# Performance work log

Measured on AMD Instinct MI355X. Metric: run time of the kernel, lower is better.

Reference implementation:

```python
import jax, jax.numpy as jnp
import numpy as np

N = 50000
E_RAND = 800000
F_IN = 128
H = 4          # num_heads
D_HID = 32     # hidden per-head dim
D_OUT = 32     # output per-head dim
NEG_SLOPE_ATTN = 0.2   # DGL GATConv attention leaky_relu
NEG_SLOPE_ACT = 0.01   # F.leaky_relu default activation


def setup_inputs() -> dict:
    key = jax.random.key(0)
    ks = jax.random.split(key, 12)
    x = jax.random.normal(ks[0], (N, F_IN), dtype=jnp.float32)
    src_r = jax.random.randint(ks[1], (E_RAND,), 0, N, dtype=jnp.int32)
    dst_r = jax.random.randint(ks[2], (E_RAND,), 0, N, dtype=jnp.int32)
    loop = jnp.arange(N, dtype=jnp.int32)
    src = jnp.concatenate([src_r, loop])  # add_self_loop
    dst = jnp.concatenate([dst_r, loop])
    sc1 = 1.0 / np.sqrt(F_IN)
    sc2 = 1.0 / np.sqrt(H * D_HID)
    W1 = jax.random.normal(ks[3], (F_IN, H * D_HID), dtype=jnp.float32) * sc1
    al1 = jax.random.normal(ks[4], (H, D_HID), dtype=jnp.float32) * sc1
    ar1 = jax.random.normal(ks[5], (H, D_HID), dtype=jnp.float32) * sc1
    b1 = jnp.zeros((H * D_HID,), dtype=jnp.float32)
    W2 = jax.random.normal(ks[6], (H * D_HID, H * D_OUT), dtype=jnp.float32) * sc2
    al2 = jax.random.normal(ks[7], (H, D_OUT), dtype=jnp.float32) * sc2
    ar2 = jax.random.normal(ks[8], (H, D_OUT), dtype=jnp.float32) * sc2
    b2 = jnp.zeros((H * D_OUT,), dtype=jnp.float32)
    return {"x": x, "src": src, "dst": dst,
            "W1": W1, "al1": al1, "ar1": ar1, "b1": b1,
            "W2": W2, "al2": al2, "ar2": ar2, "b2": b2}


def gat_conv(x, src, dst, W, al, ar, b, act_slope):
    n = x.shape[0]
    h, d = al.shape
    feat = (x @ W).reshape(n, h, d)                 # [N,H,D]
    el = jnp.einsum('nhd,hd->nh', feat, al)         # [N,H]
    er = jnp.einsum('nhd,hd->nh', feat, ar)
    # edge attention score on edge u->v: leaky_relu(el[u] + er[v])
    e = jax.nn.leaky_relu(el[src] + er[dst], NEG_SLOPE_ATTN)  # [E,H]
    # edge softmax over incoming edges of each dst node (self-loops guarantee >=1 edge)
    m = jax.ops.segment_max(e, dst, num_segments=n)           # [N,H]
    ex = jnp.exp(e - m[dst])
    s = jax.ops.segment_sum(ex, dst, num_segments=n)
    a = ex / s[dst]                                           # [E,H]
    # attention-weighted scatter-sum of source features
    out = jax.ops.segment_sum(a[:, :, None] * feat[src], dst, num_segments=n)  # [N,H,D]
    out = out + b.reshape(h, d)
    if act_slope is not None:
        out = jax.nn.leaky_relu(out, act_slope)
    return out.reshape(n, h * d)                    # flatten(1)


def reference(x, src, dst, W1, al1, ar1, b1, W2, al2, ar2, b2):
    h = gat_conv(x, src, dst, W1, al1, ar1, b1, NEG_SLOPE_ACT)
    out = gat_conv(h, src, dst, W2, al2, ar2, b2, None)  # last layer: no activation
    return out
```

## Files before the change

kernel.cpp:

```cpp
#include <hip/hip_runtime.h>
#include <hip/hip_bf16.h>
#include <hip/hip_fp16.h>

#define HEADS 4
#define DHEAD 32
#define FDIM 128
#define BCAP 64

__global__ __launch_bounds__(256) void k_gemm(
    const float* __restrict__ X, const float* __restrict__ W,
    const float* __restrict__ al, const float* __restrict__ ar,
    __half* __restrict__ feat, float* __restrict__ el, float* __restrict__ er, int n,
    const int* __restrict__ esrc, const int* __restrict__ edst,
    int* __restrict__ deg, int* __restrict__ bucket, int E) {
    __shared__ float Wl[FDIM * FDIM];
    {
        const float4* W4 = (const float4*)W;
        float4* Wl4 = (float4*)Wl;
        for (int i = threadIdx.x; i < FDIM * FDIM / 4; i += 256) Wl4[i] = W4[i];
    }

    if (E > 0) {
        int nb = gridDim.x;
        int echunk = (E + nb - 1) / nb;
        int e0 = blockIdx.x * echunk;
        int e1 = e0 + echunk; if (e1 > E) e1 = E;
        for (int base = e0 + threadIdx.x; base < e1; base += 256 * 8) {
            int d[8], s[8];
#pragma unroll
            for (int j = 0; j < 8; j++) {
                int idx = base + j * 256;
                if (idx < e1) { d[j] = edst[idx]; s[j] = esrc[idx]; }
                else d[j] = -1;
            }
#pragma unroll
            for (int j = 0; j < 8; j++) {
                if (d[j] >= 0) {
                    int p = atomicAdd(&deg[d[j]], 1);
                    if (p < BCAP) bucket[((size_t)d[j] << 6) + p] = s[j];
                }
            }
        }
    }
    __syncthreads();

    int h = __builtin_amdgcn_readfirstlane(threadIdx.x >> 6);
    int lane = threadIdx.x & 63;
    int rb = blockIdx.x * 256 + lane * 4;

    bool v[4];
    const float4* xp[4];
#pragma unroll
    for (int i = 0; i < 4; i++) {
        v[i] = (rb + i) < n;
        int cr = v[i] ? (rb + i) : (n - 1);
        xp[i] = (const float4*)(X + (size_t)cr * FDIM);
    }

    float acc[4][32];
#pragma unroll
    for (int i = 0; i < 4; i++)
#pragma unroll
        for (int j = 0; j < 32; j++) acc[i][j] = 0.f;

    const float* wbase = Wl + h * DHEAD;

    for (int k4 = 0; k4 < FDIM / 4; k4++) {
        float4 a[4];
#pragma unroll
        for (int i = 0; i < 4; i++) a[i] = xp[i][k4];
#pragma unroll
        for (int kk = 0; kk < 4; kk++) {
            const float4* wr = (const float4*)(wbase + (k4 * 4 + kk) * FDIM);
            float s[4];
#pragma unroll
            for (int i = 0; i < 4; i++) s[i] = (&a[i].x)[kk];
#pragma unroll
            for (int j4 = 0; j4 < 8; j4++) {
                float4 wv = wr[j4];
#pragma unroll
                for (int i = 0; i < 4; i++) {
                    acc[i][j4*4+0] += s[i] * wv.x;
                    acc[i][j4*4+1] += s[i] * wv.y;
                    acc[i][j4*4+2] += s[i] * wv.z;
                    acc[i][j4*4+3] += s[i] * wv.w;
                }
            }
        }
    }

    float elv[4], erv[4];
#pragma unroll
    for (int i = 0; i < 4; i++) { elv[i] = 0.f; erv[i] = 0.f; }
#pragma unroll
    for (int j = 0; j < 32; j++) {
        float va = al[h * DHEAD + j], vr = ar[h * DHEAD + j];
#pragma unroll
        for (int i = 0; i < 4; i++) {
            elv[i] += acc[i][j] * va;
            erv[i] += acc[i][j] * vr;
        }
    }
#pragma unroll
    for (int i = 0; i < 4; i++) {
        if (v[i]) {
            el[(size_t)(rb + i) * HEADS + h] = elv[i];
            er[(size_t)(rb + i) * HEADS + h] = erv[i];
        }
    }

#pragma unroll
    for (int i = 0; i < 4; i++) {
        if (!v[i]) continue;
        union { __half2 h2[16]; uint4 u4[4]; } pk;
#pragma unroll
        for (int m = 0; m < 16; m++)
            pk.h2[m] = __floats2half2_rn(acc[i][2*m], acc[i][2*m+1]);
        uint4* dstp = (uint4*)(feat + (size_t)(rb + i) * FDIM + h * DHEAD);
#pragma unroll
        for (int t = 0; t < 4; t++) dstp[t] = pk.u4[t];
    }
}

__global__ __launch_bounds__(256) void k_aggregate(
    const int* __restrict__ bucket, const int* __restrict__ deg,
    const __half2* __restrict__ feat2h, const float* __restrict__ el,
    const float* __restrict__ er, const float* __restrict__ b,
    float* __restrict__ out, int n, int apply_act) {
    int wave = threadIdx.x >> 6;
    int node = blockIdx.x * 4 + wave;
    if (node >= n) return;
    node = __builtin_amdgcn_readfirstlane(node);
    int lane = threadIdx.x & 63;
    int h = lane >> 4;

    float ern = er[(size_t)node * HEADS + h];
    int cnt = __builtin_amdgcn_readfirstlane(deg[node]);
    const int* bkt = bucket + ((size_t)node << 6);

    float ax = 0.f, ay = 0.f, sw = 0.f;
    int i = 0;

    for (; i + 8 <= cnt; i += 8) {
        int s[8];
#pragma unroll
        for (int j = 0; j < 8; j++) s[j] = bkt[i + j];
        float e[8];
#pragma unroll
        for (int j = 0; j < 8; j++) e[j] = el[(size_t)s[j] * HEADS + h];
        __half2 f[8];
#pragma unroll
        for (int j = 0; j < 8; j++) f[j] = feat2h[(size_t)s[j] * 64 + lane];
#pragma unroll
        for (int j = 0; j < 8; j++) {
            float ev = e[j] + ern;
            ev = ev > 0.f ? ev : 0.2f * ev;
            float w = __expf(ev);
            float2 fv = __half22float2(f[j]);
            sw += w; ax += w * fv.x; ay += w * fv.y;
        }
    }
    for (; i + 2 <= cnt; i += 2) {
        int s0 = bkt[i], s1 = bkt[i + 1];
        float e0 = el[(size_t)s0 * HEADS + h];
        float e1 = el[(size_t)s1 * HEADS + h];
        __half2 f0 = feat2h[(size_t)s0 * 64 + lane];
        __half2 f1 = feat2h[(size_t)s1 * 64 + lane];
        e0 += ern; e0 = e0 > 0.f ? e0 : 0.2f * e0;
        e1 += ern; e1 = e1 > 0.f ? e1 : 0.2f * e1;
        float w0 = __expf(e0), w1 = __expf(e1);
        float2 fv0 = __half22float2(f0), fv1 = __half22float2(f1);
        sw += w0 + w1;
        ax += w0 * fv0.x + w1 * fv1.x;
        ay += w0 * fv0.y + w1 * fv1.y;
    }
    if (i < cnt) {
        int s0 = bkt[i];
        float e0 = el[(size_t)s0 * HEADS + h] + ern;
        e0 = e0 > 0.f ? e0 : 0.2f * e0;
        float w0 = __expf(e0);
        float2 fv0 = __half22float2(feat2h[(size_t)s0 * 64 + lane]);
        sw += w0; ax += w0 * fv0.x; ay += w0 * fv0.y;
    }

    float inv = 1.0f / sw;
    float2 bv = ((const float2*)b)[lane];
    float ox = ax * inv + bv.x;
    float oy = ay * inv + bv.y;
    if (apply_act) {
        ox = ox > 0.f ? ox : 0.01f * ox;
        oy = oy > 0.f ? oy : 0.01f * oy;
    }
    float2 o; o.x = ox; o.y = oy;
    ((float2*)out)[(size_t)node * 64 + lane] = o;
}


extern "C" void kernel_launch(void* const* d_in, const int* in_sizes, int n_in,
                              void* d_out, int out_size, void* d_ws, size_t ws_size,
                              hipStream_t stream) {
    const float* x   = (const float*)d_in[0];
    const int*   src = (const int*)d_in[1];
    const int*   dst = (const int*)d_in[2];
    const float* W1  = (const float*)d_in[3];
    const float* al1 = (const float*)d_in[4];
    const float* ar1 = (const float*)d_in[5];
    const float* b1  = (const float*)d_in[6];
    const float* W2  = (const float*)d_in[7];
    const float* al2 = (const float*)d_in[8];
    const float* ar2 = (const float*)d_in[9];
    const float* b2  = (const float*)d_in[10];
    int N = in_sizes[0] / FDIM;
    int E = in_sizes[1];
    float* out = (float*)d_out;

    __half* featA = (__half*)d_ws;
    float* elb    = (float*)(featA + (size_t)N * FDIM);
    float* erb    = elb + (size_t)N * HEADS;
    int*   deg    = (int*)(erb + (size_t)N * HEADS);
    int*   bucket = deg + N;
    float* hbuf   = out;

    int gblocks = (N + 255) / 256;

    hipMemsetAsync(deg, 0, (size_t)N * sizeof(int), stream);

    k_gemm<<<gblocks, 256, 0, stream>>>(x, W1, al1, ar1, featA, elb, erb, N,
                                        src, dst, deg, bucket, E);
    k_aggregate<<<(N + 3) / 4, 256, 0, stream>>>(bucket, deg, (const __half2*)featA,
                                                 elb, erb, b1, hbuf, N, 1);

    k_gemm<<<gblocks, 256, 0, stream>>>(hbuf, W2, al2, ar2, featA, elb, erb, N,
                                        nullptr, nullptr, nullptr, nullptr, 0);
    k_aggregate<<<(N + 3) / 4, 256, 0, stream>>>(bucket, deg, (const __half2*)featA,
                                                 elb, erb, b2, out, N, 0);
}
```

Measured before the change: 275.5 us.

## Move edge bucketing into dedicated XCD-partitioned scatter blocks in first GEMM launch

The edge-to-bucket scatter now runs in 64 extra blocks at the start of the first GEMM grid instead of being spread across every GEMM block before its matmul. Each scatter block takes an edge slice and handles only destinations in one eighth of the node range, chosen by blockIdx&7. The intent is that atomics and bucket writes for a node range stay on one XCD's L2, and that GEMM blocks no longer wait on scatter work. The cost is that each scatter block rereads its edge slice, so edge-index traffic grows about eightfold. The speedup also depends on the assumed round-robin mapping of blocks to XCDs.

```diff
diff --git a/kernel.cpp b/kernel.cpp
--- a/kernel.cpp
+++ b/kernel.cpp
@@ -6,47 +6,53 @@
 #define DHEAD 32
 #define FDIM 128
 #define BCAP 64
+#define NSCAT 64
 
 __global__ __launch_bounds__(256) void k_gemm(
     const float* __restrict__ X, const float* __restrict__ W,
     const float* __restrict__ al, const float* __restrict__ ar,
     __half* __restrict__ feat, float* __restrict__ el, float* __restrict__ er, int n,
     const int* __restrict__ esrc, const int* __restrict__ edst,
-    int* __restrict__ deg, int* __restrict__ bucket, int E) {
+    int* __restrict__ deg, int* __restrict__ bucket, int E, int nscat) {
+
+    if (blockIdx.x < (unsigned)nscat) {
+        int xcd = blockIdx.x & 7;
+        int slice = blockIdx.x >> 3;
+        int nsl = nscat >> 3;
+        int s0 = (int)((long long)E * slice / nsl);
+        int s1 = (int)((long long)E * (slice + 1) / nsl);
+        int lo = (int)((long long)n * xcd / 8);
+        int hi = (int)((long long)n * (xcd + 1) / 8);
+        for (int base = s0 + threadIdx.x; base < s1; base += 256 * 8) {
+            int d[8], sv[8];
+#pragma unroll
+            for (int j = 0; j < 8; j++) {
+                int idx = base + j * 256;
+                d[j] = (idx < s1) ? edst[idx] : -1;
+                sv[j] = (idx < s1) ? esrc[idx] : 0;
+            }
+#pragma unroll
+            for (int j = 0; j < 8; j++) {
+                if (d[j] >= lo && d[j] < hi) {
+                    int p = atomicAdd(&deg[d[j]], 1);
+                    if (p < BCAP) bucket[((size_t)d[j] << 6) + p] = sv[j];
+                }
+            }
+        }
+        return;
+    }
+
     __shared__ float Wl[FDIM * FDIM];
     {
         const float4* W4 = (const float4*)W;
         float4* Wl4 = (float4*)Wl;
         for (int i = threadIdx.x; i < FDIM * FDIM / 4; i += 256) Wl4[i] = W4[i];
     }
-
-    if (E > 0) {
-        int nb = gridDim.x;
-        int echunk = (E + nb - 1) / nb;
-        int e0 = blockIdx.x * echunk;
-        int e1 = e0 + echunk; if (e1 > E) e1 = E;
-        for (int base = e0 + threadIdx.x; base < e1; base += 256 * 8) {
-            int d[8], s[8];
-#pragma unroll
-            for (int j = 0; j < 8; j++) {
-                int idx = base + j * 256;
-                if (idx < e1) { d[j] = edst[idx]; s[j] = esrc[idx]; }
-                else d[j] = -1;
-            }
-#pragma unroll
-            for (int j = 0; j < 8; j++) {
-                if (d[j] >= 0) {
-                    int p = atomicAdd(&deg[d[j]], 1);
-                    if (p < BCAP) bucket[((size_t)d[j] << 6) + p] = s[j];
-                }
-            }
-        }
-    }
     __syncthreads();
 
     int h = __builtin_amdgcn_readfirstlane(threadIdx.x >> 6);
     int lane = threadIdx.x & 63;
-    int rb = blockIdx.x * 256 + lane * 4;
+    int rb = (blockIdx.x - nscat) * 256 + lane * 4;
 
     bool v[4];
     const float4* xp[4];
@@ -225,13 +231,13 @@
 
     hipMemsetAsync(deg, 0, (size_t)N * sizeof(int), stream);
 
-    k_gemm<<<gblocks, 256, 0, stream>>>(x, W1, al1, ar1, featA, elb, erb, N,
-                                        src, dst, deg, bucket, E);
+    k_gemm<<<gblocks + NSCAT, 256, 0, stream>>>(x, W1, al1, ar1, featA, elb, erb, N,
+                                                src, dst, deg, bucket, E, NSCAT);
     k_aggregate<<<(N + 3) / 4, 256, 0, stream>>>(bucket, deg, (const __half2*)featA,
                                                  elb, erb, b1, hbuf, N, 1);
 
     k_gemm<<<gblocks, 256, 0, stream>>>(hbuf, W2, al2, ar2, featA, elb, erb, N,
-                                        nullptr, nullptr, nullptr, nullptr, 0);
+                                        nullptr, nullptr, nullptr, nullptr, 0, 0);
     k_aggregate<<<(N + 3) / 4, 256, 0, stream>>>(bucket, deg, (const __half2*)featA,
                                                  elb, erb, b2, out, N, 0);
 }
```

New measurement: 406.7 us. +47.6%, slower.

## Split edge scatter and layer-1 GEMM into separate block roles in one launch

Applied to the files above, without the earlier changes.

Instead of every GEMM block first doing a slice of the edge bucketing and then its GEMM rows, the first kernel now launches a fixed grid. The first nscat blocks do only the edge scatter into degree buckets, and the remaining blocks do only the GEMM. Scatter blocks skip the W load into shared memory, and both kinds of work can run concurrently on different CUs. The second-layer GEMM becomes a plain kernel with no scatter arguments. The split ratio depends on NBLK and N, and nscat is only positive while N stays below NBLK*256.

```diff
diff --git a/kernel.cpp b/kernel.cpp
--- a/kernel.cpp
+++ b/kernel.cpp
@@ -6,41 +6,132 @@
 #define DHEAD 32
 #define FDIM 128
 #define BCAP 64
-
-__global__ __launch_bounds__(256) void k_gemm(
+#define NBLK 512
+
+__global__ __launch_bounds__(256) void k_gemm1_scatter(
     const float* __restrict__ X, const float* __restrict__ W,
     const float* __restrict__ al, const float* __restrict__ ar,
     __half* __restrict__ feat, float* __restrict__ el, float* __restrict__ er, int n,
     const int* __restrict__ esrc, const int* __restrict__ edst,
-    int* __restrict__ deg, int* __restrict__ bucket, int E) {
+    int* __restrict__ deg, int* __restrict__ bucket, int E, int nscat) {
+    __shared__ float Wl[FDIM * FDIM];
+
+    if ((int)blockIdx.x < nscat) {
+        int e0 = (int)((long long)E * blockIdx.x / nscat);
+        int e1 = (int)((long long)E * (blockIdx.x + 1) / nscat);
+        for (int base = e0 + threadIdx.x; base < e1; base += 256 * 8) {
+            int d[8], sv[8];
+#pragma unroll
+            for (int j = 0; j < 8; j++) {
+                int idx = base + j * 256;
+                d[j] = (idx < e1) ? edst[idx] : -1;
+                sv[j] = (idx < e1) ? esrc[idx] : 0;
+            }
+#pragma unroll
+            for (int j = 0; j < 8; j++) {
+                if (d[j] >= 0) {
+                    int p = atomicAdd(&deg[d[j]], 1);
+                    if (p < BCAP) bucket[((size_t)d[j] << 6) + p] = sv[j];
+                }
+            }
+        }
+        return;
+    }
+
+    {
+        const float4* W4 = (const float4*)W;
+        float4* Wl4 = (float4*)Wl;
+        for (int i = threadIdx.x; i < FDIM * FDIM / 4; i += 256) Wl4[i] = W4[i];
+    }
+    __syncthreads();
+
+    int h = __builtin_amdgcn_readfirstlane(threadIdx.x >> 6);
+    int lane = threadIdx.x & 63;
+    int rb = ((int)blockIdx.x - nscat) * 256 + lane * 4;
+
+    bool v[4];
+    const float4* xp[4];
+#pragma unroll
+    for (int i = 0; i < 4; i++) {
+        v[i] = (rb + i) < n;
+        int cr = v[i] ? (rb + i) : (n - 1);
+        xp[i] = (const float4*)(X + (size_t)cr * FDIM);
+    }
+
+    float acc[4][32];
+#pragma unroll
+    for (int i = 0; i < 4; i++)
+#pragma unroll
+        for (int j = 0; j < 32; j++) acc[i][j] = 0.f;
+
+    const float* wbase = Wl + h * DHEAD;
+
+    for (int k4 = 0; k4 < FDIM / 4; k4++) {
+        float4 a[4];
+#pragma unroll
+        for (int i = 0; i < 4; i++) a[i] = xp[i][k4];
+#pragma unroll
+        for (int kk = 0; kk < 4; kk++) {
+            const float4* wr = (const float4*)(wbase + (k4 * 4 + kk) * FDIM);
+            float s[4];
+#pragma unroll
+            for (int i = 0; i < 4; i++) s[i] = (&a[i].x)[kk];
+#pragma unroll
+            for (int j4 = 0; j4 < 8; j4++) {
+                float4 wv = wr[j4];
+#pragma unroll
+                for (int i = 0; i < 4; i++) {
+                    acc[i][j4*4+0] += s[i] * wv.x;
+                    acc[i][j4*4+1] += s[i] * wv.y;
+                    acc[i][j4*4+2] += s[i] * wv.z;
+                    acc[i][j4*4+3] += s[i] * wv.w;
+                }
+            }
+        }
+    }
+
+    float elv[4], erv[4];
+#pragma unroll
+    for (int i = 0; i < 4; i++) { elv[i] = 0.f; erv[i] = 0.f; }
+#pragma unroll
+    for (int j = 0; j < 32; j++) {
+        float va = al[h * DHEAD + j], vr = ar[h * DHEAD + j];
+#pragma unroll
+        for (int i = 0; i < 4; i++) {
+            elv[i] += acc[i][j] * va;
+            erv[i] += acc[i][j] * vr;
+        }
+    }
+#pragma unroll
+    for (int i = 0; i < 4; i++) {
+        if (v[i]) {
+            el[(size_t)(rb + i) * HEADS + h] = elv[i];
+            er[(size_t)(rb + i) * HEADS + h] = erv[i];
+        }
+    }
+
+#pragma unroll
+    for (int i = 0; i < 4; i++) {
+        if (!v[i]) continue;
+        union { __half2 h2[16]; uint4 u4[4]; } pk;
+#pragma unroll
+        for (int m = 0; m < 16; m++)
+            pk.h2[m] = __floats2half2_rn(acc[i][2*m], acc[i][2*m+1]);
+        uint4* dstp = (uint4*)(feat + (size_t)(rb + i) * FDIM + h * DHEAD);
+#pragma unroll
+        for (int t = 0; t < 4; t++) dstp[t] = pk.u4[t];
+    }
+}
+
+__global__ __launch_bounds__(256) void k_gemm(
+    const float* __restrict__ X, const float* __restrict__ W,
+    const float* __restrict__ al, const float* __restrict__ ar,
+    __half* __restrict__ feat, float* __restrict__ el, float* __restrict__ er, int n) {
     __shared__ float Wl[FDIM * FDIM];
     {
         const float4* W4 = (const float4*)W;
         float4* Wl4 = (float4*)Wl;
         for (int i = threadIdx.x; i < FDIM * FDIM / 4; i += 256) Wl4[i] = W4[i];
-    }
-
-    if (E > 0) {
-        int nb = gridDim.x;
-        int echunk = (E + nb - 1) / nb;
-        int e0 = blockIdx.x * echunk;
-        int e1 = e0 + echunk; if (e1 > E) e1 = E;
-        for (int base = e0 + threadIdx.x; base < e1; base += 256 * 8) {
-            int d[8], s[8];
-#pragma unroll
-            for (int j = 0; j < 8; j++) {
-                int idx = base + j * 256;
-                if (idx < e1) { d[j] = edst[idx]; s[j] = esrc[idx]; }
-                else d[j] = -1;
-            }
-#pragma unroll
-            for (int j = 0; j < 8; j++) {
-                if (d[j] >= 0) {
-                    int p = atomicAdd(&deg[d[j]], 1);
-                    if (p < BCAP) bucket[((size_t)d[j] << 6) + p] = s[j];
-                }
-            }
-        }
     }
     __syncthreads();
 
@@ -222,16 +313,16 @@
     float* hbuf   = out;
 
     int gblocks = (N + 255) / 256;
+    int nscat = NBLK - gblocks;
 
     hipMemsetAsync(deg, 0, (size_t)N * sizeof(int), stream);
 
-    k_gemm<<<gblocks, 256, 0, stream>>>(x, W1, al1, ar1, featA, elb, erb, N,
-                                        src, dst, deg, bucket, E);
+    k_gemm1_scatter<<<NBLK, 256, 0, stream>>>(x, W1, al1, ar1, featA, elb, erb, N,
+                                              src, dst, deg, bucket, E, nscat);
     k_aggregate<<<(N + 3) / 4, 256, 0, stream>>>(bucket, deg, (const __half2*)featA,
                                                  elb, erb, b1, hbuf, N, 1);
 
-    k_gemm<<<gblocks, 256, 0, stream>>>(hbuf, W2, al2, ar2, featA, elb, erb, N,
-                                        nullptr, nullptr, nullptr, nullptr, 0);
+    k_gemm<<<gblocks, 256, 0, stream>>>(hbuf, W2, al2, ar2, featA, elb, erb, N);
     k_aggregate<<<(N + 3) / 4, 256, 0, stream>>>(bucket, deg, (const __half2*)featA,
                                                  elb, erb, b2, out, N, 0);
 }
```

New measurement: 287.6 us. 1.04x slower.
